# Kernel optimization log

Hardware: AMD Instinct MI355X
Metric: run time of the kernel (lower is better)

## Reference

```python
import jax, jax.numpy as jnp
import numpy as np

SR = 48000
TIME_LENGTH = 62400  # int(1.3 * 48000)
MAX_VOICES = 16


def _conv1d_same(x, k, b):
    # x: [B, L, Cin], k: [K, Cin, Cout] -> [B, L, Cout], keras Conv1D padding='same'
    y = jax.lax.conv_general_dilated(x, k, (1,), 'SAME', dimension_numbers=('NWC', 'WIO', 'NWC'))
    return y + b


def setup_inputs() -> dict:
    key = jax.random.key(0)
    ks = jax.random.split(key, 20)
    B, L, D, C = 16, 250, 128, 32
    V = MAX_VOICES
    din = D + C
    w = lambda k, s: jax.random.normal(k, s, jnp.float32) * 0.05
    inp = {}
    inp['base_signal'] = jax.random.normal(ks[0], (B, TIME_LENGTH), jnp.float32)
    inp['z'] = jax.random.normal(ks[1], (B, L, D), jnp.float32)
    inp['cond'] = jax.random.uniform(ks[2], (B, C), jnp.float32)
    inp['fundamental_freq'] = jax.random.uniform(ks[3], (B,), jnp.float32)
    # param_predictor: Dense(256)->Dense(128)->Dense(64)->Dense(4)
    inp['W1'] = w(ks[4], (din, 256)); inp['b1'] = jnp.zeros((256,), jnp.float32)
    inp['W2'] = w(ks[5], (256, 128)); inp['b2'] = jnp.zeros((128,), jnp.float32)
    inp['W3'] = w(ks[6], (128, 64));  inp['b3'] = jnp.zeros((64,), jnp.float32)
    inp['W4'] = w(ks[7], (64, 4));    inp['b4'] = jnp.zeros((4,), jnp.float32)
    # voice_gain_net: Conv1D(128,7)->Conv1D(64,5)->Conv1D(V,3), input channels = D + C
    inp['K1'] = w(ks[8], (7, din, 128)); inp['cb1'] = jnp.zeros((128,), jnp.float32)
    inp['K2'] = w(ks[9], (5, 128, 64));  inp['cb2'] = jnp.zeros((64,), jnp.float32)
    inp['K3'] = w(ks[10], (3, 64, V));   inp['cb3'] = jnp.zeros((V,), jnp.float32)
    return inp


def reference(base_signal, z, cond, fundamental_freq,
              W1, b1, W2, b2, W3, b3, W4, b4,
              K1, cb1, K2, cb2, K3, cb3):
    B, T = base_signal.shape
    L = z.shape[1]
    V = MAX_VOICES
    # ---- global param predictor ----
    z_global = jnp.mean(z, axis=1)
    x = jnp.concatenate([z_global, cond], axis=-1)
    h = jax.nn.relu(x @ W1 + b1)
    h = jax.nn.relu(h @ W2 + b2)
    h = jax.nn.relu(h @ W3 + b3)
    params = h @ W4 + b4  # [B,4]
    num_voices = 1.0 + 14.0 * jax.nn.sigmoid(params[:, 0:1])  # [B,1]
    detune_cents = params[:, 1:2] * 50.0                       # [B,1] (unused downstream, as in source)
    spread = jax.nn.sigmoid(params[:, 2:3])                    # [B,1]
    depth = jax.nn.sigmoid(params[:, 3:4]) * 0.5               # [B,1]
    # ---- per-voice gain envelopes at latent rate ----
    z_cond = jnp.concatenate([z, jnp.broadcast_to(cond[:, None, :], (B, L, cond.shape[-1]))], axis=-1)
    g = jax.nn.relu(_conv1d_same(z_cond, K1, cb1))
    g = jax.nn.relu(_conv1d_same(g, K2, cb2))
    g = _conv1d_same(g, K3, cb3)  # [B, L, V]
    # TF bilinear resize (half-pixel centers) L -> T along time axis
    scale = L / T
    src = jnp.clip((jnp.arange(T, dtype=jnp.float32) + 0.5) * scale - 0.5, 0.0, L - 1.0)
    i0 = jnp.floor(src).astype(jnp.int32)
    i1 = jnp.minimum(i0 + 1, L - 1)
    frac = (src - i0.astype(jnp.float32))[None, :, None]
    vg = g[:, i0, :] * (1.0 - frac) + g[:, i1, :] * frac
    voice_gains = jax.nn.softplus(vg)  # [B, T, V]
    # ---- 16-voice detune/roll/LFO-modulate/accumulate, vectorized over voices ----
    pos = (np.arange(V) - (V - 1) / 2.0) / V            # static [V]
    shifts = np.trunc(pos * 20.0).astype(np.int64)      # int() truncation as in source
    gidx = (np.arange(T)[None, :] - shifts[:, None]) % T  # static [V, T] gather for tf.roll
    shifted = base_signal[:, jnp.asarray(gidx)]         # [B, V, T]
    t = jnp.arange(T, dtype=jnp.float32) / SR
    lfo_freq = 3.0 + 0.3 * jnp.arange(V, dtype=jnp.float32)
    lfo = jnp.sin(2.0 * np.pi * lfo_freq[:, None] * t[None, :])  # [V, T]
    modulated = shifted * (1.0 + 0.2 * depth[:, 0][:, None, None] * lfo[None])  # [B, V, T]
    pan = 1.0 - jnp.abs(jnp.asarray(pos, dtype=jnp.float32))[None, :] * spread * 0.5  # [B, V]
    unison = jnp.einsum('bvt,btv,bv->bt', modulated, voice_gains, pan)  # [B, T]
    # ---- soft voice-count mask and normalization ----
    voice_mask = jax.nn.sigmoid((num_voices - jnp.arange(V, dtype=jnp.float32)[None, :]) * 2.0)  # [B, V]
    norm = jnp.sqrt(jnp.sum(voice_mask, axis=-1, keepdims=True) + 1e-6)  # [B, 1]
    gain_sum = jnp.einsum('btv,bv->bt', voice_gains, voice_mask)  # [B, T]
    return gain_sum / (norm + 1e-6) * unison
```

## Files before the change

kernel.cpp:

```cpp
#include <hip/hip_runtime.h>
#include <hip/hip_bf16.h>
#include <math.h>

#define L_LEN 250
#define D_DIM 128
#define C_DIM 32
#define DIN   160
#define NV    16
#define T_LEN 62400
#define CB    244
#define ICB1  10

__global__ __launch_bounds__(256) void conv1_mlp_kernel(
        const float* __restrict__ z, const float* __restrict__ cond,
        const float* __restrict__ K1, float* __restrict__ parts1,
        const float* __restrict__ W1, const float* __restrict__ b1,
        const float* __restrict__ W2, const float* __restrict__ b2,
        const float* __restrict__ W3, const float* __restrict__ b3,
        const float* __restrict__ W4, const float* __restrict__ b4,
        float* __restrict__ P) {
    int tid = threadIdx.x;
    __shared__ float kw[ICB1 * 7 * 128];
    __shared__ float smc[ICB1][136];

    if (blockIdx.x < 16) {
        int b = blockIdx.x;
        float* xb = kw;
        float* h1 = kw + 160;
        float* h2 = kw + 416;
        float* h3 = kw + 544;
        float* pr = kw + 608;
        float* red = kw + 640;
        float4* sm4 = (float4*)(kw + 1152);
        {
            int c4 = tid & 31, rg = tid >> 5;
            const float4* zp = (const float4*)(z + (size_t)b * L_LEN * D_DIM) + c4;
            float4 acc = make_float4(0.f, 0.f, 0.f, 0.f);
            for (int r = rg; r < L_LEN; r += 8) {
                float4 v = zp[(size_t)r * 32];
                acc.x += v.x; acc.y += v.y; acc.z += v.z; acc.w += v.w;
            }
            sm4[rg * 32 + c4] = acc;
        }
        __syncthreads();
        if (tid < 32) {
            float4 acc = sm4[tid];
            #pragma unroll
            for (int g = 1; g < 8; ++g) {
                float4 v = sm4[g * 32 + tid];
                acc.x += v.x; acc.y += v.y; acc.z += v.z; acc.w += v.w;
            }
            const float inv = 1.0f / (float)L_LEN;
            acc.x *= inv; acc.y *= inv; acc.z *= inv; acc.w *= inv;
            ((float4*)xb)[tid] = acc;
        } else if (tid >= 128 && tid < DIN) {
            xb[tid] = cond[b * C_DIM + (tid - 128)];
        }
        __syncthreads();
        {
            const float* w = W1 + tid;
            float a0 = b1[tid], a1 = 0.f, a2 = 0.f, a3 = 0.f;
            #pragma unroll 4
            for (int i = 0; i < DIN; i += 4) {
                a0 = fmaf(xb[i],     w[(size_t)(i)     * 256], a0);
                a1 = fmaf(xb[i + 1], w[(size_t)(i + 1) * 256], a1);
                a2 = fmaf(xb[i + 2], w[(size_t)(i + 2) * 256], a2);
                a3 = fmaf(xb[i + 3], w[(size_t)(i + 3) * 256], a3);
            }
            h1[tid] = fmaxf((a0 + a1) + (a2 + a3), 0.f);
        }
        __syncthreads();
        {
            int oc = tid & 127, hh = tid >> 7;
            const float* w = W2 + (size_t)(hh * 128) * 128 + oc;
            const float* x = h1 + hh * 128;
            float a0 = 0.f, a1 = 0.f, a2 = 0.f, a3 = 0.f;
            #pragma unroll 4
            for (int i = 0; i < 128; i += 4) {
                a0 = fmaf(x[i],     w[(size_t)(i)     * 128], a0);
                a1 = fmaf(x[i + 1], w[(size_t)(i + 1) * 128], a1);
                a2 = fmaf(x[i + 2], w[(size_t)(i + 2) * 128], a2);
                a3 = fmaf(x[i + 3], w[(size_t)(i + 3) * 128], a3);
            }
            red[tid] = (a0 + a1) + (a2 + a3);
        }
        __syncthreads();
        if (tid < 128) h2[tid] = fmaxf(red[tid] + red[tid + 128] + b2[tid], 0.f);
        __syncthreads();
        {
            int oc = tid & 63, qg = tid >> 6;
            const float* w = W3 + (size_t)(qg * 32) * 64 + oc;
            const float* x = h2 + qg * 32;
            float a0 = 0.f, a1 = 0.f;
            #pragma unroll 4
            for (int i = 0; i < 32; i += 2) {
                a0 = fmaf(x[i],     w[(size_t)(i)     * 64], a0);
                a1 = fmaf(x[i + 1], w[(size_t)(i + 1) * 64], a1);
            }
            red[tid] = a0 + a1;
        }
        __syncthreads();
        if (tid < 64)
            h3[tid] = fmaxf(red[tid] + red[tid + 64] + red[tid + 128] + red[tid + 192] + b3[tid], 0.f);
        __syncthreads();
        red[tid] = h3[tid >> 2] * W4[(tid >> 2) * 4 + (tid & 3)];
        __syncthreads();
        if (tid < 4) {
            float s = b4[tid];
            for (int k = 0; k < 64; ++k) s += red[k * 4 + tid];
            pr[tid] = s;
        }
        __syncthreads();
        if (tid == 0) {
            float num_voices = 1.0f + 14.0f / (1.0f + __expf(-pr[0]));
            float spread     = 1.0f / (1.0f + __expf(-pr[2]));
            float depth      = 0.5f / (1.0f + __expf(-pr[3]));
            float* Pb = P + b * 40;
            float msum = 0.f;
            for (int v = 0; v < NV; ++v) {
                float m = 1.0f / (1.0f + __expf(-(num_voices - (float)v) * 2.0f));
                msum += m;
                Pb[2 + v] = m;
                float pos = ((float)v - 7.5f) * (1.0f / 16.0f);
                Pb[2 + NV + v] = 1.0f - fabsf(pos) * spread * 0.5f;
            }
            float norm = sqrtf(msum + 1e-6f);
            Pb[0] = depth;
            Pb[1] = 1.0f / (norm + 1e-6f);
        }
        return;
    }
    int blk = blockIdx.x - 16;
    int s  = blk >> 5;
    int b  = (blk >> 1) & 15;
    int lh = blk & 1;
    int l0 = lh * 122;

    for (int idx = tid; idx < ICB1 * 7 * 128; idx += 256) {
        int oc = idx & 127;
        int r  = idx >> 7;
        int tap = r % 7, ic = r / 7;
        kw[idx] = K1[((size_t)tap * DIN + s * ICB1 + ic) * 128 + oc];
    }
    for (int idx = tid; idx < 134 * ICB1; idx += 256) {
        int ic = idx % ICB1;
        int pl = idx / ICB1;
        int p  = l0 - 3 + pl;
        int gi = s * ICB1 + ic;
        float v = 0.f;
        if (p >= 0 && p < L_LEN)
            v = (gi < D_DIM) ? z[((size_t)b * L_LEN + p) * D_DIM + gi]
                             : cond[b * C_DIM + (gi - D_DIM)];
        smc[ic][pl] = v;
    }
    __syncthreads();

    int oc0 = (tid & 31) << 2;
    int lb  = (tid >> 5) << 4;
    float acc[4][16];
    #pragma unroll
    for (int o = 0; o < 4; ++o)
        #pragma unroll
        for (int j = 0; j < 16; ++j) acc[o][j] = 0.f;

    #pragma unroll 2
    for (int ic = 0; ic < ICB1; ++ic) {
        float zr[22];
        *(float4*)&zr[0]  = *(const float4*)&smc[ic][lb];
        *(float4*)&zr[4]  = *(const float4*)&smc[ic][lb + 4];
        *(float4*)&zr[8]  = *(const float4*)&smc[ic][lb + 8];
        *(float4*)&zr[12] = *(const float4*)&smc[ic][lb + 12];
        *(float4*)&zr[16] = *(const float4*)&smc[ic][lb + 16];
        *(float2*)&zr[20] = *(const float2*)&smc[ic][lb + 20];
        const float* kwp = &kw[ic * 7 * 128 + oc0];
        #pragma unroll
        for (int tap = 0; tap < 7; ++tap) {
            float4 w = *(const float4*)(kwp + tap * 128);
            #pragma unroll
            for (int j = 0; j < 16; ++j) {
                acc[0][j] = fmaf(zr[tap + j], w.x, acc[0][j]);
                acc[1][j] = fmaf(zr[tap + j], w.y, acc[1][j]);
                acc[2][j] = fmaf(zr[tap + j], w.z, acc[2][j]);
                acc[3][j] = fmaf(zr[tap + j], w.w, acc[3][j]);
            }
        }
    }
    float* po = parts1 + (size_t)s * (16 * L_LEN * 128)
              + (size_t)b * L_LEN * 128 + oc0;
    #pragma unroll
    for (int j = 0; j < 16; ++j) {
        int l = l0 + lb + j;
        if (l < L_LEN)
            *(float4*)(po + (size_t)l * 128) =
                make_float4(acc[0][j], acc[1][j], acc[2][j], acc[3][j]);
    }
}

__global__ __launch_bounds__(256) void conv2_ws_kernel(
        const float* __restrict__ parts1, const float* __restrict__ cb1,
        const float* __restrict__ K2, float* __restrict__ parts2) {
    int tid = threadIdx.x;
    __shared__ float kw[16 * 5 * 64];
    __shared__ float smr[16][72];
    int s  = blockIdx.x >> 6;
    int b  = (blockIdx.x >> 2) & 15;
    int lt = blockIdx.x & 3;
    int l0 = lt * 62;
    const int PSTR = 16 * L_LEN * 128;

    for (int idx = tid; idx < 16 * 5 * 64; idx += 256) {
        int oc = idx & 63;
        int r  = idx >> 6;
        int tap = r % 5, ic = r / 5;
        kw[idx] = K2[((size_t)tap * 128 + s * 16 + ic) * 64 + oc];
    }
    for (int idx = tid; idx < 68 * 16; idx += 256) {
        int ch = idx & 15;
        int pl = idx >> 4;
        int p  = l0 - 2 + pl;
        int gi = s * 16 + ch;
        float v = 0.f;
        if (p >= 0 && p < L_LEN) {
            size_t o = ((size_t)b * L_LEN + p) * 128 + gi;
            float a = cb1[gi];
            #pragma unroll
            for (int k = 0; k < 16; ++k) a += parts1[o + (size_t)k * PSTR];
            v = fmaxf(a, 0.f);
        }
        smr[ch][pl] = v;
    }
    __syncthreads();

    int oc0 = (tid & 31) << 1;
    int lb  = (tid >> 5) << 3;
    float acc[2][8];
    #pragma unroll
    for (int j = 0; j < 8; ++j) { acc[0][j] = 0.f; acc[1][j] = 0.f; }

    #pragma unroll 2
    for (int ic = 0; ic < 16; ++ic) {
        float zr[12];
        *(float4*)&zr[0] = *(const float4*)&smr[ic][lb];
        *(float4*)&zr[4] = *(const float4*)&smr[ic][lb + 4];
        *(float4*)&zr[8] = *(const float4*)&smr[ic][lb + 8];
        const float* kwp = &kw[ic * 5 * 64 + oc0];
        #pragma unroll
        for (int tap = 0; tap < 5; ++tap) {
            float2 w = *(const float2*)(kwp + tap * 64);
            #pragma unroll
            for (int j = 0; j < 8; ++j) {
                acc[0][j] = fmaf(zr[tap + j], w.x, acc[0][j]);
                acc[1][j] = fmaf(zr[tap + j], w.y, acc[1][j]);
            }
        }
    }
    float* po = parts2 + (size_t)s * (16 * L_LEN * 64)
              + (size_t)b * L_LEN * 64 + oc0;
    #pragma unroll
    for (int j = 0; j < 8; ++j) {
        int l = l0 + lb + j;
        if (l < L_LEN)
            *(float2*)(po + (size_t)l * 64) = make_float2(acc[0][j], acc[1][j]);
    }
}

__global__ __launch_bounds__(256) void conv3_main_kernel(
        const float* __restrict__ base, const float* __restrict__ parts2,
        const float* __restrict__ cb2,
        const float* __restrict__ K3, const float* __restrict__ cb3,
        const float* __restrict__ P, float* __restrict__ out) {
    int b = blockIdx.x / CB;
    int c = blockIdx.x % CB;
    int t0 = c * 256;
    int tid = threadIdx.x;
    const int PSTR2 = 16 * L_LEN * 64;
    const float scale = 250.0f / 62400.0f;

    __shared__ float k3t[16][196];
    __shared__ float sA[6][68];
    __shared__ float g3loc[4][17];
    __shared__ float Pb[34];

    float src0 = ((float)t0 + 0.5f) * scale - 0.5f;
    src0 = fminf(fmaxf(src0, 0.0f), 249.0f);
    int L0 = (int)floorf(src0);

    if (tid < 34) Pb[tid] = P[b * 40 + tid];
    for (int idx = tid; idx < 3 * 64 * 16; idx += 256) {
        int v  = idx & 15;
        int ti = idx >> 4;
        k3t[v][ti] = K3[ti * 16 + v];
    }
    for (int idx = tid; idx < 6 * 64; idx += 256) {
        int pl = idx >> 6;
        int i  = idx & 63;
        int p  = L0 - 1 + pl;
        float v = 0.f;
        if (p >= 0 && p < L_LEN) {
            size_t o = ((size_t)b * L_LEN + p) * 64 + i;
            float a = cb2[i];
            #pragma unroll
            for (int k = 0; k < 8; ++k) a += parts2[o + (size_t)k * PSTR2];
            v = fmaxf(a, 0.f);
        }
        sA[pl][i] = v;
    }
    __syncthreads();

    {
        int seg = tid & 3;
        int v   = (tid >> 2) & 15;
        int r   = tid >> 6;
        float acc = 0.f;
        #pragma unroll
        for (int tap = 0; tap < 3; ++tap) {
            const float* gr = &sA[r + tap][seg * 16];
            const float* kr = &k3t[v][tap * 64 + seg * 16];
            #pragma unroll
            for (int j = 0; j < 4; ++j) {
                float4 g = *(const float4*)&gr[j * 4];
                float4 k = *(const float4*)&kr[j * 4];
                acc = fmaf(g.x, k.x, acc);
                acc = fmaf(g.y, k.y, acc);
                acc = fmaf(g.z, k.z, acc);
                acc = fmaf(g.w, k.w, acc);
            }
        }
        acc += __shfl_xor(acc, 1);
        acc += __shfl_xor(acc, 2);
        if (seg == 0) g3loc[r][v] = acc + cb3[v];
    }
    __syncthreads();

    int t = t0 + tid;
    if (t >= T_LEN) return;
    float depth = Pb[0];
    float coef  = Pb[1];
    float src = ((float)t + 0.5f) * scale - 0.5f;
    src = fminf(fmaxf(src, 0.0f), 249.0f);
    float fi0 = floorf(src);
    int i0 = (int)fi0;
    int i1 = min(i0 + 1, L_LEN - 1);
    float frac = src - fi0;
    int r0 = i0 - L0;
    int r1 = i1 - L0;
    float vg[16];
    #pragma unroll
    for (int v = 0; v < NV; ++v) {
        float a = g3loc[r0][v];
        float d = g3loc[r1][v];
        vg[v] = fmaf(d - a, frac, a);
    }
    float tsec = (float)t * (1.0f / 48000.0f);
    const float* bs = base + (size_t)b * T_LEN;
    const int shifts[NV] = {-9,-8,-6,-5,-4,-3,-1,0,0,1,3,4,5,6,8,9};
    float gain_sum = 0.f, uni = 0.f;
    #pragma unroll
    for (int v = 0; v < NV; ++v) {
        float x = vg[v];
        float sp = fmaxf(x, 0.f) + __logf(1.0f + __expf(-fabsf(x)));
        float fv = 3.0f + 0.3f * (float)v;
        float ph = fv * tsec;
        ph -= floorf(ph);
        float lfo = __builtin_amdgcn_sinf(ph);
        int tb = t - shifts[v];
        if (tb < 0) tb += T_LEN; else if (tb >= T_LEN) tb -= T_LEN;
        float mod = bs[tb] * fmaf(0.2f * depth, lfo, 1.0f);
        gain_sum = fmaf(sp, Pb[2 + v], gain_sum);
        uni      = fmaf(mod * sp, Pb[2 + NV + v], uni);
    }
    out[(size_t)b * T_LEN + t] = gain_sum * coef * uni;
}

__global__ void params_kernel(const float* __restrict__ z, const float* __restrict__ cond,
                              const float* __restrict__ W1, const float* __restrict__ b1,
                              const float* __restrict__ W2, const float* __restrict__ b2,
                              const float* __restrict__ W3, const float* __restrict__ b3,
                              const float* __restrict__ W4, const float* __restrict__ b4,
                              float* __restrict__ P) {
    int b = blockIdx.x;
    int tid = threadIdx.x;
    __shared__ float xb[DIN];
    __shared__ float zp2[128];
    __shared__ float h1[256];
    __shared__ float h2[128];
    __shared__ float h3[64];
    __shared__ float pr[4];
    {
        int i = tid & 127, half = tid >> 7;
        const float* zp = z + (size_t)b * L_LEN * D_DIM + i;
        float s = 0.f;
        for (int l = half; l < L_LEN; l += 2) s += zp[(size_t)l * D_DIM];
        if (half) zp2[i] = s;
        __syncthreads();
        if (!half) xb[i] = (s + zp2[i]) * (1.0f / (float)L_LEN);
        if (tid >= 128 && tid < DIN) xb[tid] = cond[b * C_DIM + (tid - 128)];
    }
    __syncthreads();
    {
        float acc = b1[tid];
        for (int i = 0; i < DIN; ++i) acc = fmaf(xb[i], W1[i * 256 + tid], acc);
        h1[tid] = fmaxf(acc, 0.f);
    }
    __syncthreads();
    if (tid < 128) {
        float acc = b2[tid];
        for (int i = 0; i < 256; ++i) acc = fmaf(h1[i], W2[i * 128 + tid], acc);
        h2[tid] = fmaxf(acc, 0.f);
    }
    __syncthreads();
    if (tid < 64) {
        float acc = b3[tid];
        for (int i = 0; i < 128; ++i) acc = fmaf(h2[i], W3[i * 64 + tid], acc);
        h3[tid] = fmaxf(acc, 0.f);
    }
    __syncthreads();
    if (tid < 4) {
        float acc = b4[tid];
        for (int i = 0; i < 64; ++i) acc = fmaf(h3[i], W4[i * 4 + tid], acc);
        pr[tid] = acc;
    }
    __syncthreads();
    if (tid == 0) {
        float num_voices = 1.0f + 14.0f / (1.0f + __expf(-pr[0]));
        float spread     = 1.0f / (1.0f + __expf(-pr[2]));
        float depth      = 0.5f / (1.0f + __expf(-pr[3]));
        float* Pb = P + b * 40;
        float msum = 0.f;
        for (int v = 0; v < NV; ++v) {
            float m = 1.0f / (1.0f + __expf(-(num_voices - (float)v) * 2.0f));
            msum += m;
            Pb[2 + v] = m;
            float pos = ((float)v - 7.5f) * (1.0f / 16.0f);
            Pb[2 + NV + v] = 1.0f - fabsf(pos) * spread * 0.5f;
        }
        float norm = sqrtf(msum + 1e-6f);
        Pb[0] = depth;
        Pb[1] = 1.0f / (norm + 1e-6f);
    }
}

__global__ void conv1_mono_kernel(const float* __restrict__ z, const float* __restrict__ cond,
                                  const float* __restrict__ K1, const float* __restrict__ cb1,
                                  float* __restrict__ g1) {
    int b  = blockIdx.x >> 4;
    int lt = blockIdx.x & 15;
    int l0 = lt * 16;
    int tid = threadIdx.x;
    __shared__ float sm[DIN][22];
    for (int idx = tid; idx < 22 * DIN; idx += 256) {
        int pl = idx / DIN;
        int i  = idx - pl * DIN;
        int p  = l0 - 3 + pl;
        float v = 0.f;
        if (p >= 0 && p < L_LEN)
            v = (i < D_DIM) ? z[((size_t)b * L_LEN + p) * D_DIM + i]
                            : cond[b * C_DIM + (i - D_DIM)];
        sm[i][pl] = v;
    }
    __syncthreads();
    int oc = tid & 127;
    int lb = (tid >> 7) * 8;
    float bias = cb1[oc];
    float acc[8];
    #pragma unroll
    for (int j = 0; j < 8; ++j) acc[j] = bias;
    for (int i = 0; i < DIN; ++i) {
        float zr[14];
        #pragma unroll
        for (int q = 0; q < 14; ++q) zr[q] = sm[i][lb + q];
        #pragma unroll
        for (int tap = 0; tap < 7; ++tap) {
            float k = K1[(size_t)(tap * DIN + i) * 128 + oc];
            #pragma unroll
            for (int j = 0; j < 8; ++j) acc[j] = fmaf(zr[tap + j], k, acc[j]);
        }
    }
    #pragma unroll
    for (int j = 0; j < 8; ++j) {
        int l = l0 + lb + j;
        if (l < L_LEN) g1[((size_t)b * L_LEN + l) * 128 + oc] = fmaxf(acc[j], 0.f);
    }
}

__global__ void conv2_mono_kernel(const float* __restrict__ g1,
                                  const float* __restrict__ K2, const float* __restrict__ cb2,
                                  float* __restrict__ g2) {
    int b  = blockIdx.x >> 4;
    int lt = blockIdx.x & 15;
    int l0 = lt * 16;
    int tid = threadIdx.x;
    __shared__ float sm[128][20];
    for (int idx = tid; idx < 20 * 128; idx += 256) {
        int pl = idx >> 7;
        int i  = idx & 127;
        int p  = l0 - 2 + pl;
        float v = (p >= 0 && p < L_LEN) ? g1[((size_t)b * L_LEN + p) * 128 + i] : 0.f;
        sm[i][pl] = v;
    }
    __syncthreads();
    int oc = tid & 63;
    int lb = (tid >> 6) * 4;
    float bias = cb2[oc];
    float acc[4];
    #pragma unroll
    for (int j = 0; j < 4; ++j) acc[j] = bias;
    for (int i = 0; i < 128; ++i) {
        float zr[8];
        #pragma unroll
        for (int q = 0; q < 8; ++q) zr[q] = sm[i][lb + q];
        #pragma unroll
        for (int tap = 0; tap < 5; ++tap) {
            float k = K2[(size_t)(tap * 128 + i) * 64 + oc];
            #pragma unroll
            for (int j = 0; j < 4; ++j) acc[j] = fmaf(zr[tap + j], k, acc[j]);
        }
    }
    #pragma unroll
    for (int j = 0; j < 4; ++j) {
        int l = l0 + lb + j;
        if (l < L_LEN) g2[((size_t)b * L_LEN + l) * 64 + oc] = fmaxf(acc[j], 0.f);
    }
}

__global__ void conv3_mono_kernel(const float* __restrict__ g2,
                                  const float* __restrict__ K3, const float* __restrict__ cb3,
                                  float* __restrict__ g3) {
    int b  = blockIdx.x >> 4;
    int lt = blockIdx.x & 15;
    int l0 = lt * 16;
    int tid = threadIdx.x;
    int v  = tid & 15;
    int ll = tid >> 4;
    int l  = l0 + ll;
    if (l >= L_LEN) return;
    float acc = cb3[v];
    #pragma unroll
    for (int tap = 0; tap < 3; ++tap) {
        int p = l + tap - 1;
        if (p < 0 || p >= L_LEN) continue;
        const float* gp = g2 + ((size_t)b * L_LEN + p) * 64;
        #pragma unroll
        for (int i = 0; i < 64; ++i) acc = fmaf(gp[i], K3[(size_t)(tap * 64 + i) * 16 + v], acc);
    }
    g3[((size_t)b * L_LEN + l) * 16 + v] = acc;
}

__global__ __launch_bounds__(256) void main_mono_kernel(
        const float* __restrict__ base, const float* __restrict__ g3,
        const float* __restrict__ P, float* __restrict__ out) {
    int b = blockIdx.x / CB;
    int c = blockIdx.x % CB;
    int t = c * 256 + threadIdx.x;
    __shared__ float Pb[34];
    if (threadIdx.x < 34) Pb[threadIdx.x] = P[b * 40 + threadIdx.x];
    __syncthreads();
    if (t >= T_LEN) return;
    float depth = Pb[0];
    float coef  = Pb[1];
    const float scale = 250.0f / 62400.0f;
    float src = ((float)t + 0.5f) * scale - 0.5f;
    src = fminf(fmaxf(src, 0.0f), 249.0f);
    float fi0 = floorf(src);
    int i0 = (int)fi0;
    int i1 = min(i0 + 1, L_LEN - 1);
    float frac = src - fi0;
    const float4* r0 = (const float4*)(g3 + ((size_t)b * L_LEN + i0) * NV);
    const float4* r1 = (const float4*)(g3 + ((size_t)b * L_LEN + i1) * NV);
    float vg[16];
    #pragma unroll
    for (int q = 0; q < 4; ++q) {
        float4 a = r0[q];
        float4 d = r1[q];
        vg[q * 4 + 0] = fmaf(d.x - a.x, frac, a.x);
        vg[q * 4 + 1] = fmaf(d.y - a.y, frac, a.y);
        vg[q * 4 + 2] = fmaf(d.z - a.z, frac, a.z);
        vg[q * 4 + 3] = fmaf(d.w - a.w, frac, a.w);
    }
    float tsec = (float)t * (1.0f / 48000.0f);
    const float* bs = base + (size_t)b * T_LEN;
    const int shifts[NV] = {-9,-8,-6,-5,-4,-3,-1,0,0,1,3,4,5,6,8,9};
    float gain_sum = 0.f, uni = 0.f;
    #pragma unroll
    for (int v = 0; v < NV; ++v) {
        float x = vg[v];
        float sp = fmaxf(x, 0.f) + __logf(1.0f + __expf(-fabsf(x)));
        float fv = 3.0f + 0.3f * (float)v;
        float ph = fv * tsec;
        ph -= floorf(ph);
        float lfo = __builtin_amdgcn_sinf(ph);
        int tb = t - shifts[v];
        if (tb < 0) tb += T_LEN; else if (tb >= T_LEN) tb -= T_LEN;
        float mod = bs[tb] * fmaf(0.2f * depth, lfo, 1.0f);
        gain_sum = fmaf(sp, Pb[2 + v], gain_sum);
        uni      = fmaf(mod * sp, Pb[2 + NV + v], uni);
    }
    out[(size_t)b * T_LEN + t] = gain_sum * coef * uni;
}

extern "C" void kernel_launch(void* const* d_in, const int* in_sizes, int n_in,
                              void* d_out, int out_size, void* d_ws, size_t ws_size,
                              hipStream_t stream) {
    const float* base = (const float*)d_in[0];
    const float* z    = (const float*)d_in[1];
    const float* cond = (const float*)d_in[2];
    const float* W1 = (const float*)d_in[4];  const float* b1 = (const float*)d_in[5];
    const float* W2 = (const float*)d_in[6];  const float* b2 = (const float*)d_in[7];
    const float* W3 = (const float*)d_in[8];  const float* b3 = (const float*)d_in[9];
    const float* W4 = (const float*)d_in[10]; const float* b4 = (const float*)d_in[11];
    const float* K1 = (const float*)d_in[12]; const float* cb1 = (const float*)d_in[13];
    const float* K2 = (const float*)d_in[14]; const float* cb2 = (const float*)d_in[15];
    const float* K3 = (const float*)d_in[16]; const float* cb3 = (const float*)d_in[17];
    float* out = (float*)d_out;

    int B = in_sizes[0] / T_LEN;

    float* ws = (float*)d_ws;
    const size_t P1 = (size_t)16 * L_LEN * 128;
    const size_t P2 = (size_t)16 * L_LEN * 64;
    size_t need = (1024 + 16 * P1 + 8 * P2) * sizeof(float);

    float* P = ws;
    if (ws_size >= need) {
        float* parts1 = ws + 1024;
        float* parts2 = parts1 + 16 * P1;
        conv1_mlp_kernel<<<16 + 512, 256, 0, stream>>>(
            z, cond, K1, parts1, W1, b1, W2, b2, W3, b3, W4, b4, P);
        conv2_ws_kernel<<<512, 256, 0, stream>>>(parts1, cb1, K2, parts2);
        conv3_main_kernel<<<B * CB, 256, 0, stream>>>(base, parts2, cb2, K3, cb3, P, out);
    } else {
        float* g1 = ws + 1024;
        float* g2 = g1 + (size_t)B * L_LEN * 128;
        float* g3 = g2 + (size_t)B * L_LEN * 64;
        params_kernel<<<B, 256, 0, stream>>>(z, cond, W1, b1, W2, b2, W3, b3, W4, b4, P);
        conv1_mono_kernel<<<B * 16, 256, 0, stream>>>(z, cond, K1, cb1, g1);
        conv2_mono_kernel<<<B * 16, 256, 0, stream>>>(g1, K2, cb2, g2);
        conv3_mono_kernel<<<B * 16, 256, 0, stream>>>(g2, K3, cb3, g3);
        main_mono_kernel<<<B * CB, 256, 0, stream>>>(base, g3, P, out);
    }
}
```

Measured before the change: 70.69 us.

## Replace split-K fp32 conv1 with bf16 MFMA implicit GEMM

Conv1 used to be computed as 16 split-channel fp32 FMA partial sums, written to a large partials buffer and reduced in conv2. It now runs as an implicit GEMM with bf16 16x16x32 MFMA instructions, after a new prep kernel converts the padded input and transposed K1 weights to bf16. This is meant to remove the large partials traffic and the 16-way reduction and to use matrix cores. In exchange it adds an extra kernel launch and conversion pass, and it lowers precision to bf16, which may hurt accuracy.

After: 68.76 us. -2.7%, faster.

```diff
diff --git a/kernel.cpp b/kernel.cpp
--- a/kernel.cpp
+++ b/kernel.cpp
@@ -9,29 +9,57 @@
 #define NV    16
 #define T_LEN 62400
 #define CB    244
-#define ICB1  10
-
-__global__ __launch_bounds__(256) void conv1_mlp_kernel(
+#define XROWS 272
+#define NXB   (16 * XROWS * 160)
+#define NK1   (128 * 1120)
+
+typedef short short8 __attribute__((ext_vector_type(8)));
+typedef float f32x4  __attribute__((ext_vector_type(4)));
+
+__global__ __launch_bounds__(256) void prep_kernel(
         const float* __restrict__ z, const float* __restrict__ cond,
-        const float* __restrict__ K1, float* __restrict__ parts1,
+        const float* __restrict__ K1,
+        __hip_bfloat16* __restrict__ Xb, __hip_bfloat16* __restrict__ K1t) {
+    int idx = blockIdx.x * 256 + threadIdx.x;
+    if (idx < NXB) {
+        int b   = idx / (XROWS * 160);
+        int rem = idx - b * (XROWS * 160);
+        int r   = rem / 160;
+        int ic  = rem - r * 160;
+        int l   = r - 3;
+        float v = 0.f;
+        if (l >= 0 && l < L_LEN)
+            v = (ic < D_DIM) ? z[((size_t)b * L_LEN + l) * D_DIM + ic]
+                             : cond[b * C_DIM + (ic - D_DIM)];
+        Xb[idx] = __float2bfloat16(v);
+    } else if (idx < NXB + NK1) {
+        int j  = idx - NXB;
+        int oc = j / 1120;
+        int k  = j - oc * 1120;
+        K1t[j] = __float2bfloat16(K1[(size_t)k * 128 + oc]);
+    }
+}
+
+__global__ __launch_bounds__(256) void conv1_mfma_mlp_kernel(
+        const short* __restrict__ Xb, const short* __restrict__ K1t,
+        float* __restrict__ g1,
+        const float* __restrict__ z, const float* __restrict__ cond,
         const float* __restrict__ W1, const float* __restrict__ b1,
         const float* __restrict__ W2, const float* __restrict__ b2,
         const float* __restrict__ W3, const float* __restrict__ b3,
         const float* __restrict__ W4, const float* __restrict__ b4,
         float* __restrict__ P) {
     int tid = threadIdx.x;
-    __shared__ float kw[ICB1 * 7 * 128];
-    __shared__ float smc[ICB1][136];
-
     if (blockIdx.x < 16) {
         int b = blockIdx.x;
-        float* xb = kw;
-        float* h1 = kw + 160;
-        float* h2 = kw + 416;
-        float* h3 = kw + 544;
-        float* pr = kw + 608;
-        float* red = kw + 640;
-        float4* sm4 = (float4*)(kw + 1152);
+        __shared__ float buf[2176];
+        float* xb = buf;
+        float* h1 = buf + 160;
+        float* h2 = buf + 416;
+        float* h3 = buf + 544;
+        float* pr = buf + 608;
+        float* red = buf + 640;
+        float4* sm4 = (float4*)(buf + 1152);
         {
             int c4 = tid & 31, rg = tid >> 5;
             const float4* zp = (const float4*)(z + (size_t)b * L_LEN * D_DIM) + c4;
@@ -131,73 +159,46 @@
         return;
     }
     int blk = blockIdx.x - 16;
-    int s  = blk >> 5;
-    int b  = (blk >> 1) & 15;
-    int lh = blk & 1;
-    int l0 = lh * 122;
-
-    for (int idx = tid; idx < ICB1 * 7 * 128; idx += 256) {
-        int oc = idx & 127;
-        int r  = idx >> 7;
-        int tap = r % 7, ic = r / 7;
-        kw[idx] = K1[((size_t)tap * DIN + s * ICB1 + ic) * 128 + oc];
-    }
-    for (int idx = tid; idx < 134 * ICB1; idx += 256) {
-        int ic = idx % ICB1;
-        int pl = idx / ICB1;
-        int p  = l0 - 3 + pl;
-        int gi = s * ICB1 + ic;
-        float v = 0.f;
-        if (p >= 0 && p < L_LEN)
-            v = (gi < D_DIM) ? z[((size_t)b * L_LEN + p) * D_DIM + gi]
-                             : cond[b * C_DIM + (gi - D_DIM)];
-        smc[ic][pl] = v;
-    }
-    __syncthreads();
-
-    int oc0 = (tid & 31) << 2;
-    int lb  = (tid >> 5) << 4;
-    float acc[4][16];
-    #pragma unroll
-    for (int o = 0; o < 4; ++o)
-        #pragma unroll
-        for (int j = 0; j < 16; ++j) acc[o][j] = 0.f;
-
-    #pragma unroll 2
-    for (int ic = 0; ic < ICB1; ++ic) {
-        float zr[22];
-        *(float4*)&zr[0]  = *(const float4*)&smc[ic][lb];
-        *(float4*)&zr[4]  = *(const float4*)&smc[ic][lb + 4];
-        *(float4*)&zr[8]  = *(const float4*)&smc[ic][lb + 8];
-        *(float4*)&zr[12] = *(const float4*)&smc[ic][lb + 12];
-        *(float4*)&zr[16] = *(const float4*)&smc[ic][lb + 16];
-        *(float2*)&zr[20] = *(const float2*)&smc[ic][lb + 20];
-        const float* kwp = &kw[ic * 7 * 128 + oc0];
-        #pragma unroll
-        for (int tap = 0; tap < 7; ++tap) {
-            float4 w = *(const float4*)(kwp + tap * 128);
-            #pragma unroll
-            for (int j = 0; j < 16; ++j) {
-                acc[0][j] = fmaf(zr[tap + j], w.x, acc[0][j]);
-                acc[1][j] = fmaf(zr[tap + j], w.y, acc[1][j]);
-                acc[2][j] = fmaf(zr[tap + j], w.z, acc[2][j]);
-                acc[3][j] = fmaf(zr[tap + j], w.w, acc[3][j]);
-            }
-        }
-    }
-    float* po = parts1 + (size_t)s * (16 * L_LEN * 128)
-              + (size_t)b * L_LEN * 128 + oc0;
-    #pragma unroll
-    for (int j = 0; j < 16; ++j) {
-        int l = l0 + lb + j;
-        if (l < L_LEN)
-            *(float4*)(po + (size_t)l * 128) =
-                make_float4(acc[0][j], acc[1][j], acc[2][j], acc[3][j]);
+    int b   = blk >> 4;
+    int lt  = blk & 15;
+    int l0  = lt * 16;
+    int lane = tid & 63;
+    int oc0g = (tid >> 6) * 32;
+    int m  = lane & 15;
+    int kg = lane >> 4;
+
+    const short* Ab = Xb + ((size_t)(b * XROWS + l0 + m) * 160 + kg * 8);
+    const short* Bb = K1t + ((size_t)(oc0g + m) * 1120 + kg * 8);
+
+    f32x4 acc0 = {0.f, 0.f, 0.f, 0.f};
+    f32x4 acc1 = {0.f, 0.f, 0.f, 0.f};
+    #pragma unroll 1
+    for (int tap = 0; tap < 7; ++tap) {
+        const short* ap = Ab + tap * 160;
+        const short* bp = Bb + tap * 160;
+        #pragma unroll
+        for (int ks = 0; ks < 5; ++ks) {
+            short8 av  = *(const short8*)(ap + ks * 32);
+            short8 bv0 = *(const short8*)(bp + ks * 32);
+            short8 bv1 = *(const short8*)(bp + 16 * 1120 + ks * 32);
+            acc0 = __builtin_amdgcn_mfma_f32_16x16x32_bf16(av, bv0, acc0, 0, 0, 0);
+            acc1 = __builtin_amdgcn_mfma_f32_16x16x32_bf16(av, bv1, acc1, 0, 0, 0);
+        }
+    }
+    int rbase = l0 + kg * 4;
+    #pragma unroll
+    for (int j = 0; j < 4; ++j) {
+        int lr = rbase + j;
+        if (lr < L_LEN) {
+            float* gp = g1 + ((size_t)b * L_LEN + lr) * 128 + oc0g + m;
+            gp[0]  = acc0[j];
+            gp[16] = acc1[j];
+        }
     }
 }
 
 __global__ __launch_bounds__(256) void conv2_ws_kernel(
-        const float* __restrict__ parts1, const float* __restrict__ cb1,
+        const float* __restrict__ g1, const float* __restrict__ cb1,
         const float* __restrict__ K2, float* __restrict__ parts2) {
     int tid = threadIdx.x;
     __shared__ float kw[16 * 5 * 64];
@@ -206,7 +207,6 @@
     int b  = (blockIdx.x >> 2) & 15;
     int lt = blockIdx.x & 3;
     int l0 = lt * 62;
-    const int PSTR = 16 * L_LEN * 128;
 
     for (int idx = tid; idx < 16 * 5 * 64; idx += 256) {
         int oc = idx & 63;
@@ -220,13 +220,8 @@
         int p  = l0 - 2 + pl;
         int gi = s * 16 + ch;
         float v = 0.f;
-        if (p >= 0 && p < L_LEN) {
-            size_t o = ((size_t)b * L_LEN + p) * 128 + gi;
-            float a = cb1[gi];
-            #pragma unroll
-            for (int k = 0; k < 16; ++k) a += parts1[o + (size_t)k * PSTR];
-            v = fmaxf(a, 0.f);
-        }
+        if (p >= 0 && p < L_LEN)
+            v = fmaxf(g1[((size_t)b * L_LEN + p) * 128 + gi] + cb1[gi], 0.f);
         smr[ch][pl] = v;
     }
     __syncthreads();
@@ -616,17 +611,25 @@
     int B = in_sizes[0] / T_LEN;
 
     float* ws = (float*)d_ws;
-    const size_t P1 = (size_t)16 * L_LEN * 128;
-    const size_t P2 = (size_t)16 * L_LEN * 64;
-    size_t need = (1024 + 16 * P1 + 8 * P2) * sizeof(float);
+    const size_t XBF = NXB / 2;
+    const size_t K1F = NK1 / 2;
+    const size_t G1  = (size_t)16 * L_LEN * 128;
+    const size_t P2  = (size_t)16 * L_LEN * 64;
+    size_t need = (1024 + XBF + K1F + G1 + 8 * P2) * sizeof(float);
 
     float* P = ws;
     if (ws_size >= need) {
-        float* parts1 = ws + 1024;
-        float* parts2 = parts1 + 16 * P1;
-        conv1_mlp_kernel<<<16 + 512, 256, 0, stream>>>(
-            z, cond, K1, parts1, W1, b1, W2, b2, W3, b3, W4, b4, P);
-        conv2_ws_kernel<<<512, 256, 0, stream>>>(parts1, cb1, K2, parts2);
+        __hip_bfloat16* Xb  = (__hip_bfloat16*)(ws + 1024);
+        __hip_bfloat16* K1t = (__hip_bfloat16*)(ws + 1024 + XBF);
+        float* g1     = ws + 1024 + XBF + K1F;
+        float* parts2 = g1 + G1;
+
+        int prep_blocks = (NXB + NK1 + 255) / 256;
+        prep_kernel<<<prep_blocks, 256, 0, stream>>>(z, cond, K1, Xb, K1t);
+        conv1_mfma_mlp_kernel<<<16 + 256, 256, 0, stream>>>(
+            (const short*)Xb, (const short*)K1t, g1, z, cond,
+            W1, b1, W2, b2, W3, b3, W4, b4, P);
+        conv2_ws_kernel<<<512, 256, 0, stream>>>(g1, cb1, K2, parts2);
         conv3_main_kernel<<<B * CB, 256, 0, stream>>>(base, parts2, cb2, K3, cb3, P, out);
     } else {
         float* g1 = ws + 1024;
```
